# Optimization experiments

Hardware: AMD Instinct MI355X
Metric: run time of the kernel (lower is better)

The kernel has to match this reference:

```python
import jax, jax.numpy as jnp
import numpy as np

B, S, D, E, K = 2, 2048, 512, 8, 2
H = 4 * D  # 2048


def setup_inputs() -> dict:
    key = jax.random.key(0)
    ks = jax.random.split(key, 6)
    x = jax.random.normal(ks[0], (B, S, D), dtype=jnp.float32)
    # parameters, matching torch init (randn weights, zero biases)
    w1 = jax.random.normal(ks[1], (E, D, H), dtype=jnp.float32)
    w2 = jax.random.normal(ks[2], (E, H, D), dtype=jnp.float32)
    b1 = jnp.zeros((E, H), dtype=jnp.float32)
    b2 = jnp.zeros((E, D), dtype=jnp.float32)
    # nn.Linear(D, E): kaiming-uniform-ish; plain uniform is fine for a baseline
    lim = 1.0 / np.sqrt(D)
    router_w = jax.random.uniform(ks[3], (D, E), dtype=jnp.float32, minval=-lim, maxval=lim)
    router_b = jax.random.uniform(ks[4], (E,), dtype=jnp.float32, minval=-lim, maxval=lim)
    return {"x": x, "w1": w1, "w2": w2, "b1": b1, "b2": b2,
            "router_w": router_w, "router_b": router_b}


def reference(x, w1, w2, b1, b2, router_w, router_b):
    # router: [b,s,e]
    router_logits = jnp.einsum('bsd,de->bse', x, router_w) + router_b
    top_k_logits, top_k_indices = jax.lax.top_k(router_logits, K)   # [b,s,k]
    top_k_probs = jax.nn.softmax(top_k_logits, axis=-1)             # [b,s,k]
    masks = jax.nn.one_hot(top_k_indices, E, dtype=x.dtype)          # [b,s,k,e]
    # dense all-expert MLP (faithful to source: every expert on every token)
    h = jnp.einsum('bsd,edh->bseh', x, w1) + b1                      # [b,s,e,4d]
    h = jax.nn.gelu(h, approximate=False)                            # exact gelu
    y = jnp.einsum('bseh,ehd->bsed', h, w2) + b2                     # [b,s,e,d]
    # combine: mask each expert output by routed prob and sum over top-k
    out = jnp.einsum('bsed,bske,bsk->bsd', y, masks, top_k_probs)    # [b,s,d]
    return out
```

## Files before the change

### kernel.cpp

```cpp
#include <hip/hip_runtime.h>
#include <math.h>

typedef unsigned short u16;
typedef __bf16 bf16x8 __attribute__((ext_vector_type(8)));
typedef float f32x4 __attribute__((ext_vector_type(4)));

#define T_TOKENS 4096
#define D_DIM    512
#define H_DIM    2048
#define E_NUM    8
#define CAP      4096
#define NSLOT    (T_TOKENS * 2)

__device__ __forceinline__ u16 f2bf(float f) {
  unsigned int u = __builtin_bit_cast(unsigned int, f);
  u = (u + 0x7fffu + ((u >> 16) & 1u)) >> 16;
  return (u16)u;
}

__device__ __forceinline__ void gload16(const void* g, void* l) {
  __builtin_amdgcn_global_load_lds(
      (__attribute__((address_space(1))) void*)(g),
      (__attribute__((address_space(3))) void*)(l), 16, 0, 0);
}

__device__ __forceinline__ float gelu_fast(float v) {
  float u = v * __fmaf_rn(0.071354817f, v * v, 1.59576912f);
  return v / (1.0f + __expf(-u));
}

__global__ __launch_bounds__(256) void transpose_bf16_kernel(const float* __restrict__ in,
                                                             u16* __restrict__ out,
                                                             int R, int C) {
  __shared__ float tile[64][67];
  const int e = blockIdx.z;
  const int c0 = blockIdx.x * 64, r0 = blockIdx.y * 64;
  const float* src = in + (size_t)e * R * C;
  u16* dst = out + (size_t)e * R * C;
  const int tid = threadIdx.x;
  {
    const int row = tid >> 2, cc = (tid & 3) * 16;
    const float* s = src + (size_t)(r0 + row) * C + c0 + cc;
#pragma unroll
    for (int j = 0; j < 4; j++) {
      float4 v = *(const float4*)(s + 4 * j);
      *(float4*)(&tile[row][cc + 4 * j]) = v;
    }
  }
  __syncthreads();
  {
    const int c = tid >> 2, rc = (tid & 3) * 16;
    ushort8_t: ;
    u16 buf[16];
#pragma unroll
    for (int j = 0; j < 16; j++) buf[j] = f2bf(tile[rc + j][c]);
    u16* d = dst + (size_t)(c0 + c) * R + r0 + rc;
    *(uint4*)(d) = *(uint4*)(&buf[0]);
    *(uint4*)(d + 8) = *(uint4*)(&buf[8]);
  }
}

__global__ __launch_bounds__(256) void router_kernel(const float* __restrict__ x,
                                                     const float* __restrict__ rw,
                                                     const float* __restrict__ rb,
                                                     int* __restrict__ topk_idx,
                                                     float* __restrict__ topk_p,
                                                     u16* __restrict__ xb) {
  const int lane = threadIdx.x & 63;
  const int t = blockIdx.x * 4 + (threadIdx.x >> 6);
  const float* xr = x + (size_t)t * D_DIM + lane * 8;
  float xv[8];
  *(float4*)(&xv[0]) = *(const float4*)(xr);
  *(float4*)(&xv[4]) = *(const float4*)(xr + 4);
  ushort4 o0, o1;
  o0.x = f2bf(xv[0]); o0.y = f2bf(xv[1]); o0.z = f2bf(xv[2]); o0.w = f2bf(xv[3]);
  o1.x = f2bf(xv[4]); o1.y = f2bf(xv[5]); o1.z = f2bf(xv[6]); o1.w = f2bf(xv[7]);
  ushort4* xo = (ushort4*)(xb + (size_t)t * D_DIM + lane * 8);
  xo[0] = o0; xo[1] = o1;

  float acc[8] = {0.f,0.f,0.f,0.f,0.f,0.f,0.f,0.f};
#pragma unroll
  for (int j = 0; j < 8; j++) {
    const float4* w = (const float4*)(rw + (size_t)(lane * 8 + j) * E_NUM);
    float4 w0 = w[0], w1 = w[1];
    acc[0] += xv[j] * w0.x; acc[1] += xv[j] * w0.y;
    acc[2] += xv[j] * w0.z; acc[3] += xv[j] * w0.w;
    acc[4] += xv[j] * w1.x; acc[5] += xv[j] * w1.y;
    acc[6] += xv[j] * w1.z; acc[7] += xv[j] * w1.w;
  }
#pragma unroll
  for (int off = 32; off > 0; off >>= 1) {
#pragma unroll
    for (int e = 0; e < 8; e++) acc[e] += __shfl_down(acc[e], off);
  }
  if (lane == 0) {
    float l[8];
#pragma unroll
    for (int e = 0; e < 8; e++) l[e] = acc[e] + rb[e];
    int i0 = 0; float v0 = l[0];
#pragma unroll
    for (int e = 1; e < 8; e++) if (l[e] > v0) { v0 = l[e]; i0 = e; }
    int i1 = -1; float v1 = -3.4e38f;
#pragma unroll
    for (int e = 0; e < 8; e++) if (e != i0 && l[e] > v1) { v1 = l[e]; i1 = e; }
    float p1 = expf(v1 - v0);
    float s = 1.0f + p1;
    topk_idx[t * 2] = i0; topk_idx[t * 2 + 1] = i1;
    topk_p[t * 2] = 1.0f / s; topk_p[t * 2 + 1] = p1 / s;
  }
}

__global__ __launch_bounds__(256) void compact_kernel(const int* __restrict__ topk_idx,
                                                      const float* __restrict__ topk_p,
                                                      int* __restrict__ slot_list,
                                                      float* __restrict__ prob_list,
                                                      int* __restrict__ counts) {
  const int e = blockIdx.x;
  const int tid = threadIdx.x, lane = tid & 63, w = tid >> 6;
  __shared__ int wsum[4];
  __shared__ int sbase;
  if (tid == 0) sbase = 0;
  __syncthreads();
  for (int c0 = 0; c0 < T_TOKENS; c0 += 256) {
    const int t = c0 + tid;
    const int i0 = topk_idx[t * 2], i1 = topk_idx[t * 2 + 1];
    int flag = 0, slot = 0; float p = 0.f;
    if (i0 == e)      { flag = 1; slot = t * 2;     p = topk_p[t * 2]; }
    else if (i1 == e) { flag = 1; slot = t * 2 + 1; p = topk_p[t * 2 + 1]; }
    unsigned long long m = __ballot(flag);
    if (lane == 0) wsum[w] = (int)__popcll(m);
    const int wpre = (int)__popcll(m & ((1ull << lane) - 1ull));
    __syncthreads();
    int base = sbase;
#pragma unroll
    for (int j = 0; j < 4; j++) if (j < w) base += wsum[j];
    const int tot = wsum[0] + wsum[1] + wsum[2] + wsum[3];
    if (flag) { slot_list[e * CAP + base + wpre] = slot; prob_list[e * CAP + base + wpre] = p; }
    __syncthreads();
    if (tid == 0) sbase += tot;
  }
  __syncthreads();
  if (tid == 0) counts[e] = sbase;
}

__global__ __launch_bounds__(256) void gemm1_kernel(const u16* __restrict__ xb,
                                                    const u16* __restrict__ w1t,
                                                    const float* __restrict__ b1,
                                                    const int* __restrict__ slot_list,
                                                    const float* __restrict__ prob_list,
                                                    const int* __restrict__ counts,
                                                    u16* __restrict__ hbuf) {
  const int e  = blockIdx.y >> 5;
  const int rt = blockIdx.y & 31;
  const int cnt = counts[e];
  const int rbase = rt * 128;
  if (rbase >= cnt) return;
  const int n0 = blockIdx.x * 128;

  __shared__ __align__(16) u16 At[2][128 * 64];
  __shared__ __align__(16) u16 Bt[2][128 * 64];

  const int tid = threadIdx.x, lane = tid & 63, wid = tid >> 6;
  const int wr = wid >> 1, wc = wid & 1;
  const int lr8 = lane >> 3;
  const int sx = lane & 7;
  const int kperm = (sx ^ lr8) * 8;
  const int lrow = lane & 15, lk = lane >> 4;

  const u16* pa[4]; const u16* pb[4]; int lo[4];
#pragma unroll
  for (int i = 0; i < 4; i++) {
    const int row = (wid * 4 + i) * 8 + lr8;
    const int grow = rbase + row;
    int tok = 0;
    if (grow < cnt) tok = slot_list[e * CAP + grow] >> 1;
    pa[i] = xb + (size_t)tok * D_DIM + kperm;
    pb[i] = w1t + ((size_t)e * H_DIM + n0 + row) * D_DIM + kperm;
    lo[i] = (wid * 4 + i) * 512;
  }

  f32x4 acc[4][4];
#pragma unroll
  for (int i = 0; i < 4; i++)
#pragma unroll
    for (int j = 0; j < 4; j++) acc[i][j] = (f32x4){0.f, 0.f, 0.f, 0.f};

  auto stage = [&](int k0, int b) {
#pragma unroll
    for (int i = 0; i < 4; i++) gload16(pa[i] + k0, &At[b][lo[i]]);
#pragma unroll
    for (int i = 0; i < 4; i++) gload16(pb[i] + k0, &Bt[b][lo[i]]);
  };

  stage(0, 0);
  stage(64, 1);
  const int nt = D_DIM / 64;
#pragma unroll
  for (int t = 0; t < nt; ++t) {
    const int cur = t & 1;
    if (t < nt - 1) { asm volatile("s_waitcnt vmcnt(8)" ::: "memory"); }
    else            { asm volatile("s_waitcnt vmcnt(0)" ::: "memory"); }
    __builtin_amdgcn_sched_barrier(0);
    __builtin_amdgcn_s_barrier();
    bf16x8 afr[4][2], bfr[4][2];
#pragma unroll
    for (int ks = 0; ks < 2; ks++)
#pragma unroll
      for (int f = 0; f < 4; f++) {
        afr[f][ks] = *(const bf16x8*)(&At[cur][(wr * 64 + f * 16 + lrow) * 64 + ((ks * 4 + lk) ^ sx) * 8]);
        bfr[f][ks] = *(const bf16x8*)(&Bt[cur][(wc * 64 + f * 16 + lrow) * 64 + ((ks * 4 + lk) ^ sx) * 8]);
      }
    asm volatile("s_waitcnt lgkmcnt(0)" ::: "memory");
    __builtin_amdgcn_sched_barrier(0);
    __builtin_amdgcn_s_barrier();
    if (t + 2 < nt) stage((t + 2) * 64, cur);
    __builtin_amdgcn_sched_barrier(0);
    __builtin_amdgcn_s_setprio(1);
#pragma unroll
    for (int ks = 0; ks < 2; ks++)
#pragma unroll
      for (int fr = 0; fr < 4; fr++)
#pragma unroll
        for (int fc = 0; fc < 4; fc++)
          acc[fr][fc] = __builtin_amdgcn_mfma_f32_16x16x32_bf16(afr[fr][ks], bfr[fc][ks], acc[fr][fc], 0, 0, 0);
    __builtin_amdgcn_s_setprio(0);
  }

  float bias[4];
#pragma unroll
  for (int fc = 0; fc < 4; fc++) bias[fc] = b1[e * H_DIM + n0 + wc * 64 + fc * 16 + lrow];
#pragma unroll
  for (int fr = 0; fr < 4; fr++) {
#pragma unroll
    for (int reg = 0; reg < 4; reg++) {
      const int rloc = wr * 64 + fr * 16 + lk * 4 + reg;
      const int grow = rbase + rloc;
      if (grow < cnt) {
        const int slot = slot_list[e * CAP + grow];
        const float p  = prob_list[e * CAP + grow];
        u16* dst = hbuf + (size_t)slot * H_DIM + n0 + wc * 64 + lrow;
#pragma unroll
        for (int fc = 0; fc < 4; fc++) {
          float v = acc[fr][fc][reg] + bias[fc];
          dst[fc * 16] = f2bf(gelu_fast(v) * p);
        }
      }
    }
  }
}

__global__ __launch_bounds__(256) void gemm2_kernel(const u16* __restrict__ hbuf,
                                                    const u16* __restrict__ w2t,
                                                    const float* __restrict__ b2,
                                                    const int* __restrict__ slot_list,
                                                    const float* __restrict__ prob_list,
                                                    const int* __restrict__ counts,
                                                    float* __restrict__ ypart) {
  const int e  = blockIdx.y >> 6;
  const int rt = blockIdx.y & 63;
  const int s  = blockIdx.z;
  const int cnt = counts[e];
  const int rbase = rt * 64;
  if (rbase >= cnt) return;
  const int n0 = blockIdx.x * 128;
  const int kb = s * (H_DIM / 2);

  __shared__ __align__(16) u16 At[2][64 * 64];
  __shared__ __align__(16) u16 Bt[2][128 * 64];

  const int tid = threadIdx.x, lane = tid & 63, wid = tid >> 6;
  const int wr = wid >> 1, wc = wid & 1;
  const int lr8 = lane >> 3;
  const int sx = lane & 7;
  const int kperm = (sx ^ lr8) * 8;
  const int lrow = lane & 15, lk = lane >> 4;

  const u16* pa[2]; int loa[2];
#pragma unroll
  for (int i = 0; i < 2; i++) {
    const int row = (wid * 2 + i) * 8 + lr8;
    const int grow = rbase + row;
    int slot = 0;
    if (grow < cnt) slot = slot_list[e * CAP + grow];
    pa[i] = hbuf + (size_t)slot * H_DIM + kb + kperm;
    loa[i] = (wid * 2 + i) * 512;
  }
  const u16* pb[4]; int lob[4];
#pragma unroll
  for (int i = 0; i < 4; i++) {
    const int row = (wid * 4 + i) * 8 + lr8;
    pb[i] = w2t + ((size_t)e * D_DIM + n0 + row) * H_DIM + kb + kperm;
    lob[i] = (wid * 4 + i) * 512;
  }

  f32x4 acc[2][4];
#pragma unroll
  for (int i = 0; i < 2; i++)
#pragma unroll
    for (int j = 0; j < 4; j++) acc[i][j] = (f32x4){0.f, 0.f, 0.f, 0.f};

  auto stage = [&](int k0, int b) {
#pragma unroll
    for (int i = 0; i < 2; i++) gload16(pa[i] + k0, &At[b][loa[i]]);
#pragma unroll
    for (int i = 0; i < 4; i++) gload16(pb[i] + k0, &Bt[b][lob[i]]);
  };

  stage(0, 0);
  stage(64, 1);
  const int nt = (H_DIM / 2) / 64;
#pragma unroll
  for (int t = 0; t < nt; ++t) {
    const int cur = t & 1;
    if (t < nt - 1) { asm volatile("s_waitcnt vmcnt(6)" ::: "memory"); }
    else            { asm volatile("s_waitcnt vmcnt(0)" ::: "memory"); }
    __builtin_amdgcn_sched_barrier(0);
    __builtin_amdgcn_s_barrier();
    bf16x8 afr[2][2], bfr[4][2];
#pragma unroll
    for (int ks = 0; ks < 2; ks++) {
#pragma unroll
      for (int f = 0; f < 2; f++)
        afr[f][ks] = *(const bf16x8*)(&At[cur][(wr * 32 + f * 16 + lrow) * 64 + ((ks * 4 + lk) ^ sx) * 8]);
#pragma unroll
      for (int f = 0; f < 4; f++)
        bfr[f][ks] = *(const bf16x8*)(&Bt[cur][(wc * 64 + f * 16 + lrow) * 64 + ((ks * 4 + lk) ^ sx) * 8]);
    }
    asm volatile("s_waitcnt lgkmcnt(0)" ::: "memory");
    __builtin_amdgcn_sched_barrier(0);
    __builtin_amdgcn_s_barrier();
    if (t + 2 < nt) stage((t + 2) * 64, cur);
    __builtin_amdgcn_sched_barrier(0);
    __builtin_amdgcn_s_setprio(1);
#pragma unroll
    for (int ks = 0; ks < 2; ks++)
#pragma unroll
      for (int fr = 0; fr < 2; fr++)
#pragma unroll
        for (int fc = 0; fc < 4; fc++)
          acc[fr][fc] = __builtin_amdgcn_mfma_f32_16x16x32_bf16(afr[fr][ks], bfr[fc][ks], acc[fr][fc], 0, 0, 0);
    __builtin_amdgcn_s_setprio(0);
  }

#pragma unroll
  for (int fr = 0; fr < 2; fr++) {
#pragma unroll
    for (int reg = 0; reg < 4; reg++) {
      const int rloc = wr * 32 + fr * 16 + lk * 4 + reg;
      const int grow = rbase + rloc;
      if (grow < cnt) {
        const int slot = slot_list[e * CAP + grow];
        const float p  = prob_list[e * CAP + grow];
        float* dst = ypart + ((size_t)s * NSLOT + slot) * D_DIM + n0 + wc * 64 + lrow;
#pragma unroll
        for (int fc = 0; fc < 4; fc++) {
          float v = acc[fr][fc][reg];
          if (s == 0) v += p * b2[e * D_DIM + n0 + wc * 64 + fc * 16 + lrow];
          dst[fc * 16] = v;
        }
      }
    }
  }
}

__global__ __launch_bounds__(256) void combine_kernel(const float* __restrict__ yp,
                                                      float* __restrict__ out) {
  int i = blockIdx.x * 256 + threadIdx.x;
  int t = i >> 7;
  int dq = i & 127;
  float4 a = ((const float4*)(yp + (size_t)(t * 2) * D_DIM))[dq];
  float4 b = ((const float4*)(yp + (size_t)(t * 2 + 1) * D_DIM))[dq];
  float4 c = ((const float4*)(yp + ((size_t)NSLOT + t * 2) * D_DIM))[dq];
  float4 d = ((const float4*)(yp + ((size_t)NSLOT + t * 2 + 1) * D_DIM))[dq];
  float4 r;
  r.x = a.x + b.x + c.x + d.x;
  r.y = a.y + b.y + c.y + d.y;
  r.z = a.z + b.z + c.z + d.z;
  r.w = a.w + b.w + c.w + d.w;
  ((float4*)(out + (size_t)t * D_DIM))[dq] = r;
}

extern "C" void kernel_launch(void* const* d_in, const int* in_sizes, int n_in,
                              void* d_out, int out_size, void* d_ws, size_t ws_size,
                              hipStream_t stream) {
  const float* x  = (const float*)d_in[0];
  const float* w1 = (const float*)d_in[1];
  const float* w2 = (const float*)d_in[2];
  const float* b1 = (const float*)d_in[3];
  const float* b2 = (const float*)d_in[4];
  const float* rw = (const float*)d_in[5];
  const float* rb = (const float*)d_in[6];
  float* out = (float*)d_out;

  char* ws = (char*)d_ws;
  size_t off = 0;
  auto alloc = [&](size_t bytes) -> void* {
    void* p = ws + off;
    off = (off + bytes + 255) & ~(size_t)255;
    return p;
  };
  int*   counts    = (int*)alloc(E_NUM * 4);
  int*   slot_list = (int*)alloc((size_t)E_NUM * CAP * 4);
  float* prob_list = (float*)alloc((size_t)E_NUM * CAP * 4);
  int*   topk_idx  = (int*)alloc((size_t)T_TOKENS * 2 * 4);
  float* topk_p    = (float*)alloc((size_t)T_TOKENS * 2 * 4);
  u16*   xb        = (u16*)alloc((size_t)T_TOKENS * D_DIM * 2);
  u16*   w1t       = (u16*)alloc((size_t)E_NUM * H_DIM * D_DIM * 2);
  u16*   w2t       = (u16*)alloc((size_t)E_NUM * H_DIM * D_DIM * 2);
  u16*   hbuf      = (u16*)alloc((size_t)NSLOT * H_DIM * 2);
  float* ypart     = (float*)alloc((size_t)2 * NSLOT * D_DIM * 4);

  transpose_bf16_kernel<<<dim3(H_DIM / 64, D_DIM / 64, E_NUM), 256, 0, stream>>>(w1, w1t, D_DIM, H_DIM);
  transpose_bf16_kernel<<<dim3(D_DIM / 64, H_DIM / 64, E_NUM), 256, 0, stream>>>(w2, w2t, H_DIM, D_DIM);
  router_kernel<<<T_TOKENS / 4, 256, 0, stream>>>(x, rw, rb, topk_idx, topk_p, xb);
  compact_kernel<<<E_NUM, 256, 0, stream>>>(topk_idx, topk_p, slot_list, prob_list, counts);
  gemm1_kernel<<<dim3(H_DIM / 128, E_NUM * 32), 256, 0, stream>>>(xb, w1t, b1, slot_list, prob_list, counts, hbuf);
  gemm2_kernel<<<dim3(D_DIM / 128, E_NUM * 64, 2), 256, 0, stream>>>(hbuf, w2t, b2, slot_list, prob_list, counts, ypart);
  combine_kernel<<<(T_TOKENS * D_DIM / 4) / 256, 256, 0, stream>>>(ypart, out);
}
```

Measured before the change: 136.3 us.

## Fuse weight transposes, drop split-K and combine kernel via atomic accumulation

```diff
diff --git a/kernel.cpp b/kernel.cpp
--- a/kernel.cpp
+++ b/kernel.cpp
@@ -26,36 +26,41 @@
 
 __device__ __forceinline__ float gelu_fast(float v) {
   float u = v * __fmaf_rn(0.071354817f, v * v, 1.59576912f);
-  return v / (1.0f + __expf(-u));
-}
-
-__global__ __launch_bounds__(256) void transpose_bf16_kernel(const float* __restrict__ in,
-                                                             u16* __restrict__ out,
-                                                             int R, int C) {
+  float e = __expf(-u);
+  return v * __builtin_amdgcn_rcpf(1.0f + e);
+}
+
+__global__ __launch_bounds__(256) void transpose_both_kernel(const float* __restrict__ w1,
+                                                             const float* __restrict__ w2,
+                                                             u16* __restrict__ w1t,
+                                                             u16* __restrict__ w2t) {
   __shared__ float tile[64][67];
-  const int e = blockIdx.z;
-  const int c0 = blockIdx.x * 64, r0 = blockIdx.y * 64;
-  const float* src = in + (size_t)e * R * C;
-  u16* dst = out + (size_t)e * R * C;
+  int bid = blockIdx.x;
+  const float* in; u16* out; int R, C;
+  if (bid < 2048) { in = w1; out = w1t; R = D_DIM; C = H_DIM; }
+  else            { bid -= 2048; in = w2; out = w2t; R = H_DIM; C = D_DIM; }
+  const int e = bid >> 8;
+  const int t = bid & 255;
+  const int nCx = C >> 6;
+  const int c0 = (t % nCx) * 64, r0 = (t / nCx) * 64;
+  const float* src = in + (size_t)e * D_DIM * H_DIM;
+  u16* dst = out + (size_t)e * D_DIM * H_DIM;
   const int tid = threadIdx.x;
   {
     const int row = tid >> 2, cc = (tid & 3) * 16;
     const float* s = src + (size_t)(r0 + row) * C + c0 + cc;
 #pragma unroll
-    for (int j = 0; j < 4; j++) {
-      float4 v = *(const float4*)(s + 4 * j);
-      *(float4*)(&tile[row][cc + 4 * j]) = v;
-    }
+    for (int j = 0; j < 4; j++)
+      *(float4*)(&tile[row][cc + 4 * j]) = *(const float4*)(s + 4 * j);
   }
   __syncthreads();
   {
     const int c = tid >> 2, rc = (tid & 3) * 16;
-    ushort8_t: ;
     u16 buf[16];
 #pragma unroll
     for (int j = 0; j < 16; j++) buf[j] = f2bf(tile[rc + j][c]);
     u16* d = dst + (size_t)(c0 + c) * R + r0 + rc;
-    *(uint4*)(d) = *(uint4*)(&buf[0]);
+    *(uint4*)(d)     = *(uint4*)(&buf[0]);
     *(uint4*)(d + 8) = *(uint4*)(&buf[8]);
   }
 }
@@ -65,7 +70,14 @@
                                                      const float* __restrict__ rb,
                                                      int* __restrict__ topk_idx,
                                                      float* __restrict__ topk_p,
-                                                     u16* __restrict__ xb) {
+                                                     u16* __restrict__ xb,
+                                                     float* __restrict__ outz) {
+  {
+    float4 z = {0.f, 0.f, 0.f, 0.f};
+    float4* o = (float4*)(outz + (size_t)blockIdx.x * 2048);
+    o[threadIdx.x] = z;
+    o[threadIdx.x + 256] = z;
+  }
   const int lane = threadIdx.x & 63;
   const int t = blockIdx.x * 4 + (threadIdx.x >> 6);
   const float* xr = x + (size_t)t * D_DIM + lane * 8;
@@ -143,13 +155,13 @@
   if (tid == 0) counts[e] = sbase;
 }
 
-__global__ __launch_bounds__(256) void gemm1_kernel(const u16* __restrict__ xb,
-                                                    const u16* __restrict__ w1t,
-                                                    const float* __restrict__ b1,
-                                                    const int* __restrict__ slot_list,
-                                                    const float* __restrict__ prob_list,
-                                                    const int* __restrict__ counts,
-                                                    u16* __restrict__ hbuf) {
+__global__ __launch_bounds__(256, 2) void gemm1_kernel(const u16* __restrict__ xb,
+                                                       const u16* __restrict__ w1t,
+                                                       const float* __restrict__ b1,
+                                                       const int* __restrict__ slot_list,
+                                                       const float* __restrict__ prob_list,
+                                                       const int* __restrict__ counts,
+                                                       u16* __restrict__ hbuf) {
   const int e  = blockIdx.y >> 5;
   const int rt = blockIdx.y & 31;
   const int cnt = counts[e];
@@ -249,21 +261,19 @@
   }
 }
 
-__global__ __launch_bounds__(256) void gemm2_kernel(const u16* __restrict__ hbuf,
-                                                    const u16* __restrict__ w2t,
-                                                    const float* __restrict__ b2,
-                                                    const int* __restrict__ slot_list,
-                                                    const float* __restrict__ prob_list,
-                                                    const int* __restrict__ counts,
-                                                    float* __restrict__ ypart) {
+__global__ __launch_bounds__(256, 3) void gemm2_kernel(const u16* __restrict__ hbuf,
+                                                       const u16* __restrict__ w2t,
+                                                       const float* __restrict__ b2,
+                                                       const int* __restrict__ slot_list,
+                                                       const float* __restrict__ prob_list,
+                                                       const int* __restrict__ counts,
+                                                       float* __restrict__ out) {
   const int e  = blockIdx.y >> 6;
   const int rt = blockIdx.y & 63;
-  const int s  = blockIdx.z;
   const int cnt = counts[e];
   const int rbase = rt * 64;
   if (rbase >= cnt) return;
   const int n0 = blockIdx.x * 128;
-  const int kb = s * (H_DIM / 2);
 
   __shared__ __align__(16) u16 At[2][64 * 64];
   __shared__ __align__(16) u16 Bt[2][128 * 64];
@@ -282,14 +292,14 @@
     const int grow = rbase + row;
     int slot = 0;
     if (grow < cnt) slot = slot_list[e * CAP + grow];
-    pa[i] = hbuf + (size_t)slot * H_DIM + kb + kperm;
+    pa[i] = hbuf + (size_t)slot * H_DIM + kperm;
     loa[i] = (wid * 2 + i) * 512;
   }
   const u16* pb[4]; int lob[4];
 #pragma unroll
   for (int i = 0; i < 4; i++) {
     const int row = (wid * 4 + i) * 8 + lr8;
-    pb[i] = w2t + ((size_t)e * D_DIM + n0 + row) * H_DIM + kb + kperm;
+    pb[i] = w2t + ((size_t)e * D_DIM + n0 + row) * H_DIM + kperm;
     lob[i] = (wid * 4 + i) * 512;
   }
 
@@ -308,8 +318,8 @@
 
   stage(0, 0);
   stage(64, 1);
-  const int nt = (H_DIM / 2) / 64;
-#pragma unroll
+  const int nt = H_DIM / 64;
+#pragma unroll 2
   for (int t = 0; t < nt; ++t) {
     const int cur = t & 1;
     if (t < nt - 1) { asm volatile("s_waitcnt vmcnt(6)" ::: "memory"); }
@@ -351,33 +361,15 @@
       if (grow < cnt) {
         const int slot = slot_list[e * CAP + grow];
         const float p  = prob_list[e * CAP + grow];
-        float* dst = ypart + ((size_t)s * NSLOT + slot) * D_DIM + n0 + wc * 64 + lrow;
+        float* dst = out + (size_t)(slot >> 1) * D_DIM + n0 + wc * 64 + lrow;
 #pragma unroll
         for (int fc = 0; fc < 4; fc++) {
-          float v = acc[fr][fc][reg];
-          if (s == 0) v += p * b2[e * D_DIM + n0 + wc * 64 + fc * 16 + lrow];
-          dst[fc * 16] = v;
+          float v = acc[fr][fc][reg] + p * b2[e * D_DIM + n0 + wc * 64 + fc * 16 + lrow];
+          atomicAdd(&dst[fc * 16], v);
         }
       }
     }
   }
-}
-
-__global__ __launch_bounds__(256) void combine_kernel(const float* __restrict__ yp,
-                                                      float* __restrict__ out) {
-  int i = blockIdx.x * 256 + threadIdx.x;
-  int t = i >> 7;
-  int dq = i & 127;
-  float4 a = ((const float4*)(yp + (size_t)(t * 2) * D_DIM))[dq];
-  float4 b = ((const float4*)(yp + (size_t)(t * 2 + 1) * D_DIM))[dq];
-  float4 c = ((const float4*)(yp + ((size_t)NSLOT + t * 2) * D_DIM))[dq];
-  float4 d = ((const float4*)(yp + ((size_t)NSLOT + t * 2 + 1) * D_DIM))[dq];
-  float4 r;
-  r.x = a.x + b.x + c.x + d.x;
-  r.y = a.y + b.y + c.y + d.y;
-  r.z = a.z + b.z + c.z + d.z;
-  r.w = a.w + b.w + c.w + d.w;
-  ((float4*)(out + (size_t)t * D_DIM))[dq] = r;
 }
 
 extern "C" void kernel_launch(void* const* d_in, const int* in_sizes, int n_in,
@@ -408,13 +400,10 @@
   u16*   w1t       = (u16*)alloc((size_t)E_NUM * H_DIM * D_DIM * 2);
   u16*   w2t       = (u16*)alloc((size_t)E_NUM * H_DIM * D_DIM * 2);
   u16*   hbuf      = (u16*)alloc((size_t)NSLOT * H_DIM * 2);
-  float* ypart     = (float*)alloc((size_t)2 * NSLOT * D_DIM * 4);
-
-  transpose_bf16_kernel<<<dim3(H_DIM / 64, D_DIM / 64, E_NUM), 256, 0, stream>>>(w1, w1t, D_DIM, H_DIM);
-  transpose_bf16_kernel<<<dim3(D_DIM / 64, H_DIM / 64, E_NUM), 256, 0, stream>>>(w2, w2t, H_DIM, D_DIM);
-  router_kernel<<<T_TOKENS / 4, 256, 0, stream>>>(x, rw, rb, topk_idx, topk_p, xb);
+
+  transpose_both_kernel<<<4096, 256, 0, stream>>>(w1, w2, w1t, w2t);
+  router_kernel<<<T_TOKENS / 4, 256, 0, stream>>>(x, rw, rb, topk_idx, topk_p, xb, out);
   compact_kernel<<<E_NUM, 256, 0, stream>>>(topk_idx, topk_p, slot_list, prob_list, counts);
   gemm1_kernel<<<dim3(H_DIM / 128, E_NUM * 32), 256, 0, stream>>>(xb, w1t, b1, slot_list, prob_list, counts, hbuf);
-  gemm2_kernel<<<dim3(D_DIM / 128, E_NUM * 64, 2), 256, 0, stream>>>(hbuf, w2t, b2, slot_list, prob_list, counts, ypart);
-  combine_kernel<<<(T_TOKENS * D_DIM / 4) / 256, 256, 0, stream>>>(ypart, out);
-}
+  gemm2_kernel<<<dim3(D_DIM / 128, E_NUM * 64), 256, 0, stream>>>(hbuf, w2t, b2, slot_list, prob_list, counts, out);
+}
```

Measured after the change: 129.0 us. -5.3%, faster.
